# Kernel tuning notes

Hardware: AMD Instinct MI355X
Metric: run time of the kernel (lower is better)

The kernel has to match this reference:

```python
import jax, jax.numpy as jnp
import numpy as np

PS = 14            # patch size
EMBED = 1024       # vision embed dim
LLM = 2048         # llm embed dim
DS = 2             # downsample factor
B = 8
GRID = 64          # H = W = 64 patches per image
MAX_POS = 4096
ROPE_THETA = 10000.0


def _rope_cache(dim, max_pos, base):
    inv_freq = 1.0 / (base ** (jnp.arange(0, dim, 2, dtype=jnp.float32) / dim))
    t = jnp.arange(max_pos, dtype=jnp.float32)
    freqs = jnp.outer(t, inv_freq)  # [max_pos, dim//2]
    return jnp.cos(freqs), jnp.sin(freqs)


def setup_inputs() -> dict:
    key = jax.random.key(0)
    ks = jax.random.split(key, 5)
    n_total = B * GRID * GRID
    pixel_values = jax.random.normal(ks[0], (n_total, 3, PS, PS), jnp.float32)
    patch_w = jax.random.normal(ks[1], (EMBED, 3, PS, PS), jnp.float32) * (1.0 / np.sqrt(3 * PS * PS))
    patch_b = jax.random.normal(ks[2], (EMBED,), jnp.float32) * 0.02
    dense_w = jax.random.normal(ks[3], (LLM, EMBED, DS, DS), jnp.float32) * (1.0 / np.sqrt(EMBED * DS * DS))
    dense_b = jax.random.normal(ks[4], (LLM,), jnp.float32) * 0.02
    rope_dim = EMBED // 2
    cos_x, sin_x = _rope_cache(rope_dim, MAX_POS, ROPE_THETA)
    cos_y, sin_y = _rope_cache(rope_dim, MAX_POS, ROPE_THETA)
    grid_hw = jnp.full((B, 2), GRID, dtype=jnp.int32)
    return {"pixel_values": pixel_values, "grid_hw": grid_hw,
            "patch_w": patch_w, "patch_b": patch_b,
            "dense_w": dense_w, "dense_b": dense_b,
            "cos_x": cos_x, "sin_x": sin_x, "cos_y": cos_y, "sin_y": sin_y}


def _apply_rotary_1d(x, cos_c, sin_c, pos):
    # x: [N, d], cos_c/sin_c: [max_pos, d//2], pos: [N] int
    c = cos_c[pos]  # gather: [N, d//2]
    s = sin_c[pos]
    x1 = x[:, 0::2]
    x2 = x[:, 1::2]
    o1 = x1 * c - x2 * s
    o2 = x1 * s + x2 * c
    return jnp.stack([o1, o2], axis=-1).reshape(x.shape)  # re-interleave


def _positions(grid_np):
    # grid metadata is static host-side data; build per-patch (x, y) coords
    xs, ys = [], []
    for h, w in grid_np:
        pid = np.arange(h * w)
        xs.append(pid % w)
        ys.append(pid // w)
    return jnp.asarray(np.concatenate(xs)), jnp.asarray(np.concatenate(ys))


def reference(pixel_values, grid_hw, patch_w, patch_b, dense_w, dense_b,
              cos_x, sin_x, cos_y, sin_y):
    grid_np = np.asarray(grid_hw)
    # patchify conv (kernel == stride == patch) is a per-patch linear proj
    pe = jnp.einsum('nchw,echw->ne', pixel_values, patch_w) + patch_b  # [N, E]
    pe = jax.nn.gelu(pe, approximate=False)
    abs_x, abs_y = _positions(grid_np)
    half = EMBED // 2
    p1 = _apply_rotary_1d(pe[:, :half], cos_x, sin_x, abs_x)
    p2 = _apply_rotary_1d(pe[:, half:], cos_y, sin_y, abs_y)
    pe = jnp.concatenate([p1, p2], axis=-1)  # [N, E]
    # per-image downsample conv (kernel == stride == DS): 2x2 block linear
    outs = []
    cur = 0
    for h, w in grid_np:
        x = pe[cur:cur + h * w].reshape(h // DS, DS, w // DS, DS, EMBED)
        o = jnp.einsum('hpwqe,oepq->hwo', x, dense_w) + dense_b
        outs.append(o.reshape(-1, LLM))
        cur += h * w
    return jnp.concatenate(outs, axis=0)
```

## Files before the change

kernel.cpp:

```cpp
#include <hip/hip_runtime.h>
#include <cstdint>


using f16x8 = __attribute__((ext_vector_type(8))) _Float16;
using f32x4 = __attribute__((ext_vector_type(4))) float;

__device__ __forceinline__ void gload_lds16(const void* g, void* l) {
  __builtin_amdgcn_global_load_lds(
      reinterpret_cast<const __attribute__((address_space(1))) unsigned int*>(
          reinterpret_cast<uintptr_t>(g)),
      reinterpret_cast<__attribute__((address_space(3))) unsigned int*>(
          reinterpret_cast<uintptr_t>(l)),
      16, 0, 0);
}

__device__ __forceinline__ f16x8 ldsr(unsigned addr) {
  f16x8 r;
  asm volatile("ds_read_b128 %0, %1" : "=v"(r) : "v"(addr));
  return r;
}


#define KP 640

__global__ void conv_b1_kernel(const float* __restrict__ w1,
                               _Float16* __restrict__ h) {
  int i = blockIdx.x * 256 + threadIdx.x;
  if (i >= 1024 * KP) return;
  int e = i / KP;
  int k = i - e * KP;
  float v = (k < 588) ? w1[(size_t)e * 588 + k] : 0.0f;
  h[i] = (_Float16)v;
}

__global__ void conv_b2_kernel(const float* __restrict__ w2,
                               _Float16* __restrict__ h) {
  int i = blockIdx.x * 256 + threadIdx.x;
  int o   = i >> 12;
  int rem = i & 4095;
  int pq  = rem >> 10;
  int e   = rem & 1023;
  h[i] = (_Float16)w2[(size_t)o * 4096 + e * 4 + pq];
}

__global__ void conv_pix_kernel(const float* __restrict__ pix,
                                _Float16* __restrict__ h) {
  int i = blockIdx.x * 256 + threadIdx.x;
  if (i >= 32768 * (KP / 8)) return;
  int n = i / (KP / 8);
  int g = i - n * (KP / 8);
  int k0 = g * 8;
  f16x8 v;
  if (k0 + 8 <= 588) {
    const float4 x0 = *(const float4*)(pix + (size_t)n * 588 + k0);
    const float4 x1 = *(const float4*)(pix + (size_t)n * 588 + k0 + 4);
    v[0] = (_Float16)x0.x; v[1] = (_Float16)x0.y;
    v[2] = (_Float16)x0.z; v[3] = (_Float16)x0.w;
    v[4] = (_Float16)x1.x; v[5] = (_Float16)x1.y;
    v[6] = (_Float16)x1.z; v[7] = (_Float16)x1.w;
  } else {
#pragma unroll
    for (int j = 0; j < 8; ++j) {
      int k = k0 + j;
      v[j] = (k < 588) ? (_Float16)pix[(size_t)n * 588 + k] : (_Float16)0.0f;
    }
  }
  *(f16x8*)(h + (size_t)n * KP + k0) = v;
}


#define BAR   asm volatile("s_barrier" ::: "memory")
#define LGKM0 do { asm volatile("s_waitcnt lgkmcnt(0)" ::: "memory");         \
                   __builtin_amdgcn_sched_barrier(0); } while (0)
#define V6  asm volatile("s_waitcnt vmcnt(6)" ::: "memory")
#define V4  asm volatile("s_waitcnt vmcnt(4)" ::: "memory")
#define V0  asm volatile("s_waitcnt vmcnt(0)" ::: "memory")
#define VN  ((void)0)

#define MM16(I0, J0, AV, BV)                                                  \
  _Pragma("unroll") for (int i_ = 0; i_ < 4; ++i_)                            \
  _Pragma("unroll") for (int j_ = 0; j_ < 2; ++j_)                            \
  _Pragma("unroll") for (int ks_ = 0; ks_ < 2; ++ks_)                         \
      acc[(I0) + i_][(J0) + j_] = __builtin_amdgcn_mfma_f32_16x16x32_f16(     \
          AV[i_][ks_], BV[j_][ks_], acc[(I0) + i_][(J0) + j_], 0, 0, 0);

#define TILE_ITER(s, DOA, DOB, STGA, STGB, DRA, DRB, DRC, DRD)                \
  {                                                                           \
    const unsigned dbase = base + ((unsigned)((s) & 1) << 16);                \
    f16x8 av[4][2], vb0[2][2], vb1[2][2];                                     \
                                                       \
    _Pragma("unroll") for (int i = 0; i < 4; ++i) {                           \
      av[i][0] = ldsr(dbase + aoffs + (unsigned)(i * 2048) + soff0);          \
      av[i][1] = ldsr(dbase + aoffs + (unsigned)(i * 2048) + soff1);          \
    }                                                                         \
    _Pragma("unroll") for (int j = 0; j < 2; ++j) {                           \
      vb0[j][0] = ldsr(dbase + boffs + (unsigned)(j * 2048) + soff0);         \
      vb0[j][1] = ldsr(dbase + boffs + (unsigned)(j * 2048) + soff1);         \
    }                                                                         \
    if (DOA) STGA(0, (s) + 1);                                                \
    BAR; LGKM0;                                                               \
    __builtin_amdgcn_s_setprio(1);                                            \
    MM16(0, 0, av, vb0);                                                      \
    __builtin_amdgcn_s_setprio(0);                                            \
    DRA; BAR;                                                                 \
                                                       \
    _Pragma("unroll") for (int j = 0; j < 2; ++j) {                           \
      vb1[j][0] = ldsr(dbase + boffs + (unsigned)((2 + j) * 2048) + soff0);   \
      vb1[j][1] = ldsr(dbase + boffs + (unsigned)((2 + j) * 2048) + soff1);   \
    }                                                                         \
    if (DOA) STGA(1, (s) + 1);                                                \
    BAR; LGKM0;                                                               \
    __builtin_amdgcn_s_setprio(1);                                            \
    MM16(0, 2, av, vb1);                                                      \
    __builtin_amdgcn_s_setprio(0);                                            \
    DRB; BAR;                                                                 \
                                                       \
    _Pragma("unroll") for (int i = 0; i < 4; ++i) {                           \
      av[i][0] = ldsr(dbase + aoffs + (unsigned)((4 + i) * 2048) + soff0);    \
      av[i][1] = ldsr(dbase + aoffs + (unsigned)((4 + i) * 2048) + soff1);    \
    }                                                                         \
    if (DOB) STGB(0, (s) + 2);                                                \
    BAR; LGKM0;                                                               \
    __builtin_amdgcn_s_setprio(1);                                            \
    MM16(4, 2, av, vb1);                                                      \
    __builtin_amdgcn_s_setprio(0);                                            \
    DRC; BAR;                                                                 \
                                                       \
    if (DOB) STGB(1, (s) + 2);                                                \
    BAR;                                                                      \
    __builtin_amdgcn_s_setprio(1);                                            \
    MM16(4, 0, av, vb0);                                                      \
    __builtin_amdgcn_s_setprio(0);                                            \
    DRD; BAR;                                                                 \
  }


#define P_STGA(h, s)                                                          \
  _Pragma("unroll") for (int u = 0; u < 2; ++u) {                             \
    const int ibase = wave * 64 + u * 512;                                    \
    const int i = ibase + lane;                                               \
    const int row = i >> 3;                                                   \
    const int m = bm256 + (h) * 128 + row;                                    \
    const int gcol = (i & 7) ^ (row & 7);                                     \
    gload_lds16(pixf + (size_t)m * KP + (s) * 64 + gcol * 8,                  \
                (char*)lds + (((s) & 1) * 65536 + (h) * 16384 + ibase * 16)); \
  }
#define P_STGB(h, s)                                                          \
  _Pragma("unroll") for (int u = 0; u < 2; ++u) {                             \
    const int ibase = wave * 64 + u * 512;                                    \
    const int i = ibase + lane;                                               \
    const int row = i >> 3;                                                   \
    const int e = bn * 256 + (h) * 128 + row;                                 \
    const int gcol = (i & 7) ^ (row & 7);                                     \
    gload_lds16(b1w + (size_t)e * KP + (s) * 64 + gcol * 8,                   \
                (char*)lds + (((s) & 1) * 65536 + (2 + (h)) * 16384 +         \
                              ibase * 16));                                   \
  }

__global__ __launch_bounds__(512, 2) void patch_gemm8(
    const _Float16* __restrict__ pixf,
    const _Float16* __restrict__ b1w,
    const float* __restrict__ bias1,
    const float* __restrict__ cosx, const float* __restrict__ sinx,
    const float* __restrict__ cosy, const float* __restrict__ siny,
    _Float16* __restrict__ pe)
{
  __shared__ _Float16 lds[2][4][128][64];

  const int tid  = threadIdx.x;
  const int lane = tid & 63;
  const int wave = tid >> 6;
  const int wm = wave >> 2;
  const int wn = wave & 3;
  const int bm = blockIdx.x, bn = blockIdx.y;
  const int l15 = lane & 15;
  const int g   = lane >> 4;
  const int s7  = l15 & 7;

  const unsigned base  = (unsigned)(uintptr_t)&lds[0][0][0][0];
  const unsigned aoffs = (unsigned)(wm * 16384 + l15 * 128);
  const unsigned boffs = (unsigned)(32768 + (wn >> 1) * 16384 +
                                    (wn & 1) * 8192 + l15 * 128);
  const unsigned soff0 = (unsigned)(((0 + g) ^ s7) * 16);
  const unsigned soff1 = (unsigned)(((4 + g) ^ s7) * 16);

  const int bm256 = bm * 256;

  f32x4 acc[8][4] = {};

  P_STGA(0, 0); P_STGA(1, 0); P_STGB(0, 0); P_STGB(1, 0);
  P_STGB(0, 1); P_STGB(1, 1);
  V0; BAR;

  for (int kt = 0; kt < 8; ++kt)
    TILE_ITER(kt, 1, 1, P_STGA, P_STGB, V6, V6, V6, V4);
  TILE_ITER(8, 1, 0, P_STGA, P_STGB, V6, V6, V6, V0);
  TILE_ITER(9, 0, 0, P_STGA, P_STGB, VN, VN, VN, VN);

  const int md = (lane >> 4) * 4;
#pragma unroll
  for (int mf = 0; mf < 8; ++mf) {
#pragma unroll
    for (int r = 0; r < 4; ++r) {
      const int m = bm256 + wm * 128 + mf * 16 + md + r;
      const int pid  = m & 4095;
      const int posx = pid & 63;
      const int posy = (pid >> 6) & 63;
#pragma unroll
      for (int nf = 0; nf < 4; ++nf) {
        const int e = bn * 256 + wn * 64 + nf * 16 + l15;
        float v = acc[mf][nf][r] + bias1[e];
        v = 0.5f * v * (1.0f + erff(v * 0.70710678118654752f));
        const float pv = __shfl_xor(v, 1, 64);
        const int h2  = (e >= 512) ? 1 : 0;
        const int idx = (h2 ? (e - 512) : e) >> 1;
        const int pos = h2 ? posy : posx;
        const float cc = (h2 ? cosy : cosx)[pos * 256 + idx];
        const float ss = (h2 ? siny : sinx)[pos * 256 + idx];
        const float o = ((lane & 1) == 0) ? (v * cc - pv * ss)
                                          : (pv * ss + v * cc);
        pe[(size_t)m * 1024 + e] = (_Float16)o;
      }
    }
  }
}


#define D_STGA(h, s)                                                          \
  {                                                                           \
    const int pq = (s) >> 4, p = pq >> 1, q = pq & 1;                         \
    const int e0 = ((s) & 15) << 6;                                           \
    _Pragma("unroll") for (int u = 0; u < 2; ++u) {                           \
      const int ibase = wave * 64 + u * 512;                                  \
      const int i = ibase + lane;                                             \
      const int row = i >> 3;                                                 \
      const int t_ = bm256 + (h) * 128 + row;                                 \
      const int rr = t_ & 1023;                                               \
      const int prow =                                                        \
          (t_ >> 10) * 4096 + ((rr >> 5) * 2 + p) * 64 + (rr & 31) * 2 + q;   \
      const int gcol = (i & 7) ^ (row & 7);                                   \
      gload_lds16(pe + (size_t)prow * 1024 + e0 + gcol * 8,                   \
                  (char*)lds + (((s) & 1) * 65536 + (h) * 16384 +             \
                                ibase * 16));                                 \
    }                                                                         \
  }
#define D_STGB(h, s)                                                          \
  _Pragma("unroll") for (int u = 0; u < 2; ++u) {                             \
    const int ibase = wave * 64 + u * 512;                                    \
    const int i = ibase + lane;                                               \
    const int row = i >> 3;                                                   \
    const int n = bn * 256 + (h) * 128 + row;                                 \
    const int gcol = (i & 7) ^ (row & 7);                                     \
    gload_lds16(b2w + (size_t)n * 4096 + (s) * 64 + gcol * 8,                 \
                (char*)lds + (((s) & 1) * 65536 + (2 + (h)) * 16384 +         \
                              ibase * 16));                                   \
  }

__global__ __launch_bounds__(512, 2) void dense_gemm8(
    const _Float16* __restrict__ pe,
    const _Float16* __restrict__ b2w,
    const float* __restrict__ bias2, float* __restrict__ out)
{
  __shared__ _Float16 lds[2][4][128][64];

  const int tid  = threadIdx.x;
  const int lane = tid & 63;
  const int wave = tid >> 6;
  const int wm = wave >> 2;
  const int wn = wave & 3;
  const int f   = blockIdx.x;
  const int swz = (f & 7) * 32 + (f >> 3);
  const int bm  = swz & 31;
  const int bn  = swz >> 5;
  const int l15 = lane & 15;
  const int g   = lane >> 4;
  const int s7  = l15 & 7;

  const unsigned base  = (unsigned)(uintptr_t)&lds[0][0][0][0];
  const unsigned aoffs = (unsigned)(wm * 16384 + l15 * 128);
  const unsigned boffs = (unsigned)(32768 + (wn >> 1) * 16384 +
                                    (wn & 1) * 8192 + l15 * 128);
  const unsigned soff0 = (unsigned)(((0 + g) ^ s7) * 16);
  const unsigned soff1 = (unsigned)(((4 + g) ^ s7) * 16);

  const int bm256 = bm * 256;

  f32x4 acc[8][4] = {};

  D_STGA(0, 0); D_STGA(1, 0); D_STGB(0, 0); D_STGB(1, 0);
  D_STGB(0, 1); D_STGB(1, 1);
  V0; BAR;

  for (int kt = 0; kt < 62; ++kt)
    TILE_ITER(kt, 1, 1, D_STGA, D_STGB, V6, V6, V6, V4);
  TILE_ITER(62, 1, 0, D_STGA, D_STGB, V6, V6, V6, V0);
  TILE_ITER(63, 0, 0, D_STGA, D_STGB, VN, VN, VN, VN);

  const int md = (lane >> 4) * 4;
  const int r0 = bm256 + wm * 128;
  const int c0 = bn * 256 + wn * 64;
#pragma unroll
  for (int nf = 0; nf < 4; ++nf) {
    const int o = c0 + nf * 16 + l15;
    const float bs = bias2[o];
#pragma unroll
    for (int mf = 0; mf < 8; ++mf) {
      const int t_ = r0 + mf * 16 + md;
#pragma unroll
      for (int r = 0; r < 4; ++r)
        out[(size_t)(t_ + r) * 2048 + o] = acc[mf][nf][r] + bs;
    }
  }
}


extern "C" void kernel_launch(void* const* d_in, const int* in_sizes, int n_in,
                              void* d_out, int out_size, void* d_ws, size_t ws_size,
                              hipStream_t stream) {
  const float* pix  = (const float*)d_in[0];
  const float* w1   = (const float*)d_in[2];
  const float* b1   = (const float*)d_in[3];
  const float* w2   = (const float*)d_in[4];
  const float* b2   = (const float*)d_in[5];
  const float* cosx = (const float*)d_in[6];
  const float* sinx = (const float*)d_in[7];
  const float* cosy = (const float*)d_in[8];
  const float* siny = (const float*)d_in[9];
  float* out = (float*)d_out;

  _Float16* ws = (_Float16*)d_ws;
  const size_t PE_N  = (size_t)32768 * 1024;
  const size_t B1_N  = (size_t)1024 * KP;
  const size_t B2_N  = (size_t)2048 * 4096;
  _Float16* peb  = ws;
  _Float16* b1h  = peb + PE_N;
  _Float16* b2h  = b1h + B1_N;
  _Float16* pixf = b2h + B2_N;

  conv_b1_kernel<<<dim3((1024 * KP + 255) / 256), dim3(256), 0, stream>>>(w1, b1h);
  conv_b2_kernel<<<dim3(32768), dim3(256), 0, stream>>>(w2, b2h);
  conv_pix_kernel<<<dim3((32768 * (KP / 8) + 255) / 256), dim3(256), 0, stream>>>(pix, pixf);
  patch_gemm8<<<dim3(128, 4), dim3(512), 0, stream>>>(
      pixf, b1h, b1, cosx, sinx, cosy, siny, peb);
  dense_gemm8<<<dim3(256), dim3(512), 0, stream>>>(
      peb, b2h, b2, out);
}
```

Before: 303.1 us.

## Simplify GEMM pipelines and write patch embeddings in dense-gemm layout

Both GEMM kernels drop the hand-scheduled four-phase loop with partial vmcnt waits and interleaved staging. They now use a simple double-buffered loop that issues the next stage's loads, runs all MFMAs, then does a full wait and barrier. The patch GEMM epilogue scatters its output straight into the 2x2-downsample layout ([token][pq*1024+e]), so the dense GEMM reads A contiguously instead of through gathered row indices. The dense grid's block swizzle is removed as well. The loss of fine-grained load/compute overlap and L2-friendly block ordering may outweigh the cheaper addressing.

Result: faster. 290.8 us (-4.1%).

```diff
diff --git a/kernel.cpp b/kernel.cpp
--- a/kernel.cpp
+++ b/kernel.cpp
@@ -14,14 +14,12 @@
       16, 0, 0);
 }
 
-__device__ __forceinline__ f16x8 ldsr(unsigned addr) {
-  f16x8 r;
-  asm volatile("ds_read_b128 %0, %1" : "=v"(r) : "v"(addr));
-  return r;
-}
-
+#define BAR   asm volatile("s_barrier" ::: "memory")
+#define LGKM0 asm volatile("s_waitcnt lgkmcnt(0)" ::: "memory")
+#define VM0   asm volatile("s_waitcnt vmcnt(0)" ::: "memory")
 
 #define KP 640
+
 
 __global__ void conv_b1_kernel(const float* __restrict__ w1,
                                _Float16* __restrict__ h) {
@@ -69,133 +67,96 @@
 }
 
 
-#define BAR   asm volatile("s_barrier" ::: "memory")
-#define LGKM0 do { asm volatile("s_waitcnt lgkmcnt(0)" ::: "memory");         \
-                   __builtin_amdgcn_sched_barrier(0); } while (0)
-#define V6  asm volatile("s_waitcnt vmcnt(6)" ::: "memory")
-#define V4  asm volatile("s_waitcnt vmcnt(4)" ::: "memory")
-#define V0  asm volatile("s_waitcnt vmcnt(0)" ::: "memory")
-#define VN  ((void)0)
-
-#define MM16(I0, J0, AV, BV)                                                  \
+#define MFMA16(I0, J0, AV, BV)                                                \
   _Pragma("unroll") for (int i_ = 0; i_ < 4; ++i_)                            \
   _Pragma("unroll") for (int j_ = 0; j_ < 2; ++j_)                            \
-  _Pragma("unroll") for (int ks_ = 0; ks_ < 2; ++ks_)                         \
+  _Pragma("unroll") for (int k_ = 0; k_ < 2; ++k_)                            \
       acc[(I0) + i_][(J0) + j_] = __builtin_amdgcn_mfma_f32_16x16x32_f16(     \
-          AV[i_][ks_], BV[j_][ks_], acc[(I0) + i_][(J0) + j_], 0, 0, 0);
-
-#define TILE_ITER(s, DOA, DOB, STGA, STGB, DRA, DRB, DRC, DRD)                \
+          AV[i_][k_], BV[j_][k_], acc[(I0) + i_][(J0) + j_], 0, 0, 0);
+
+#define TILE_BODY(sb)                                                         \
   {                                                                           \
-    const unsigned dbase = base + ((unsigned)((s) & 1) << 16);                \
-    f16x8 av[4][2], vb0[2][2], vb1[2][2];                                     \
-                                                       \
+    f16x8 a0[4][2], a1[4][2], vb0[2][2], vb1[2][2];                           \
     _Pragma("unroll") for (int i = 0; i < 4; ++i) {                           \
-      av[i][0] = ldsr(dbase + aoffs + (unsigned)(i * 2048) + soff0);          \
-      av[i][1] = ldsr(dbase + aoffs + (unsigned)(i * 2048) + soff1);          \
+      a0[i][0] = *(const f16x8*)(lbase + (sb) + aoff + i * 2048 + so0);       \
+      a0[i][1] = *(const f16x8*)(lbase + (sb) + aoff + i * 2048 + so1);       \
     }                                                                         \
     _Pragma("unroll") for (int j = 0; j < 2; ++j) {                           \
-      vb0[j][0] = ldsr(dbase + boffs + (unsigned)(j * 2048) + soff0);         \
-      vb0[j][1] = ldsr(dbase + boffs + (unsigned)(j * 2048) + soff1);         \
-    }                                                                         \
-    if (DOA) STGA(0, (s) + 1);                                                \
-    BAR; LGKM0;                                                               \
-    __builtin_amdgcn_s_setprio(1);                                            \
-    MM16(0, 0, av, vb0);                                                      \
-    __builtin_amdgcn_s_setprio(0);                                            \
-    DRA; BAR;                                                                 \
-                                                       \
+      vb0[j][0] = *(const f16x8*)(lbase + (sb) + boff + j * 2048 + so0);      \
+      vb0[j][1] = *(const f16x8*)(lbase + (sb) + boff + j * 2048 + so1);      \
+    }                                                                         \
+    MFMA16(0, 0, a0, vb0);                                                    \
     _Pragma("unroll") for (int j = 0; j < 2; ++j) {                           \
-      vb1[j][0] = ldsr(dbase + boffs + (unsigned)((2 + j) * 2048) + soff0);   \
-      vb1[j][1] = ldsr(dbase + boffs + (unsigned)((2 + j) * 2048) + soff1);   \
-    }                                                                         \
-    if (DOA) STGA(1, (s) + 1);                                                \
-    BAR; LGKM0;                                                               \
-    __builtin_amdgcn_s_setprio(1);                                            \
-    MM16(0, 2, av, vb1);                                                      \
-    __builtin_amdgcn_s_setprio(0);                                            \
-    DRB; BAR;                                                                 \
-                                                       \
+      vb1[j][0] = *(const f16x8*)(lbase + (sb) + boff + (2+j) * 2048 + so0);  \
+      vb1[j][1] = *(const f16x8*)(lbase + (sb) + boff + (2+j) * 2048 + so1);  \
+    }                                                                         \
+    MFMA16(0, 2, a0, vb1);                                                    \
     _Pragma("unroll") for (int i = 0; i < 4; ++i) {                           \
-      av[i][0] = ldsr(dbase + aoffs + (unsigned)((4 + i) * 2048) + soff0);    \
-      av[i][1] = ldsr(dbase + aoffs + (unsigned)((4 + i) * 2048) + soff1);    \
-    }                                                                         \
-    if (DOB) STGB(0, (s) + 2);                                                \
-    BAR; LGKM0;                                                               \
-    __builtin_amdgcn_s_setprio(1);                                            \
-    MM16(4, 2, av, vb1);                                                      \
-    __builtin_amdgcn_s_setprio(0);                                            \
-    DRC; BAR;                                                                 \
-                                                       \
-    if (DOB) STGB(1, (s) + 2);                                                \
-    BAR;                                                                      \
-    __builtin_amdgcn_s_setprio(1);                                            \
-    MM16(4, 0, av, vb0);                                                      \
-    __builtin_amdgcn_s_setprio(0);                                            \
-    DRD; BAR;                                                                 \
-  }
-
-
-#define P_STGA(h, s)                                                          \
-  _Pragma("unroll") for (int u = 0; u < 2; ++u) {                             \
-    const int ibase = wave * 64 + u * 512;                                    \
-    const int i = ibase + lane;                                               \
-    const int row = i >> 3;                                                   \
-    const int m = bm256 + (h) * 128 + row;                                    \
-    const int gcol = (i & 7) ^ (row & 7);                                     \
-    gload_lds16(pixf + (size_t)m * KP + (s) * 64 + gcol * 8,                  \
-                (char*)lds + (((s) & 1) * 65536 + (h) * 16384 + ibase * 16)); \
-  }
-#define P_STGB(h, s)                                                          \
-  _Pragma("unroll") for (int u = 0; u < 2; ++u) {                             \
-    const int ibase = wave * 64 + u * 512;                                    \
-    const int i = ibase + lane;                                               \
-    const int row = i >> 3;                                                   \
-    const int e = bn * 256 + (h) * 128 + row;                                 \
-    const int gcol = (i & 7) ^ (row & 7);                                     \
-    gload_lds16(b1w + (size_t)e * KP + (s) * 64 + gcol * 8,                   \
-                (char*)lds + (((s) & 1) * 65536 + (2 + (h)) * 16384 +         \
-                              ibase * 16));                                   \
-  }
-
-__global__ __launch_bounds__(512, 2) void patch_gemm8(
+      a1[i][0] = *(const f16x8*)(lbase + (sb) + aoff + (4+i) * 2048 + so0);   \
+      a1[i][1] = *(const f16x8*)(lbase + (sb) + aoff + (4+i) * 2048 + so1);   \
+    }                                                                         \
+    MFMA16(4, 2, a1, vb1);                                                    \
+    MFMA16(4, 0, a1, vb0);                                                    \
+  }
+
+
+__global__ __launch_bounds__(512, 2) void patch_gemm9(
     const _Float16* __restrict__ pixf,
     const _Float16* __restrict__ b1w,
     const float* __restrict__ bias1,
     const float* __restrict__ cosx, const float* __restrict__ sinx,
     const float* __restrict__ cosy, const float* __restrict__ siny,
-    _Float16* __restrict__ pe)
+    _Float16* __restrict__ peM)
 {
-  __shared__ _Float16 lds[2][4][128][64];
+  __shared__ _Float16 lds[2][2][256][64];
 
   const int tid  = threadIdx.x;
   const int lane = tid & 63;
   const int wave = tid >> 6;
-  const int wm = wave >> 2;
-  const int wn = wave & 3;
+  const int wm = wave >> 2, wn = wave & 3;
   const int bm = blockIdx.x, bn = blockIdx.y;
   const int l15 = lane & 15;
   const int g   = lane >> 4;
   const int s7  = l15 & 7;
 
-  const unsigned base  = (unsigned)(uintptr_t)&lds[0][0][0][0];
-  const unsigned aoffs = (unsigned)(wm * 16384 + l15 * 128);
-  const unsigned boffs = (unsigned)(32768 + (wn >> 1) * 16384 +
-                                    (wn & 1) * 8192 + l15 * 128);
-  const unsigned soff0 = (unsigned)(((0 + g) ^ s7) * 16);
-  const unsigned soff1 = (unsigned)(((4 + g) ^ s7) * 16);
-
-  const int bm256 = bm * 256;
+  const char* lbase = (const char*)lds;
+  char*       lw    = (char*)lds;
+  const unsigned aoff = (unsigned)(wm * 16384 + l15 * 128);
+  const unsigned boff = (unsigned)(32768 + wn * 8192 + l15 * 128);
+  const unsigned so0  = (unsigned)(((0 + g) ^ s7) * 16);
+  const unsigned so1  = (unsigned)(((4 + g) ^ s7) * 16);
+
+  const int bm256 = bm * 256, bn256 = bn * 256;
+  const int srow = (wave * 4) * 8 + (lane >> 3);
+  const int sgc  = (lane & 7) ^ (srow & 7);
+
+  auto STAGE = [&](int s) {
+    char* slot = lw + ((size_t)(s & 1) << 16);
+    const int c0 = s * 64;
+#pragma unroll
+    for (int u = 0; u < 4; ++u) {
+      const int row  = srow + u * 8;
+      const int gcol = (lane & 7) ^ (row & 7);
+      gload_lds16(pixf + (size_t)(bm256 + row) * KP + c0 + gcol * 8,
+                  slot + (wave * 4 + u) * 1024);
+      gload_lds16(b1w + (size_t)(bn256 + row) * KP + c0 + gcol * 8,
+                  slot + 32768 + (wave * 4 + u) * 1024);
+    }
+  };
+  (void)sgc;
 
   f32x4 acc[8][4] = {};
 
-  P_STGA(0, 0); P_STGA(1, 0); P_STGB(0, 0); P_STGB(1, 0);
-  P_STGB(0, 1); P_STGB(1, 1);
-  V0; BAR;
-
-  for (int kt = 0; kt < 8; ++kt)
-    TILE_ITER(kt, 1, 1, P_STGA, P_STGB, V6, V6, V6, V4);
-  TILE_ITER(8, 1, 0, P_STGA, P_STGB, V6, V6, V6, V0);
-  TILE_ITER(9, 0, 0, P_STGA, P_STGB, VN, VN, VN, VN);
+  STAGE(0); VM0; BAR;
+#pragma unroll 2
+  for (int s = 0; s < 10; ++s) {
+    if (s + 1 < 10) STAGE(s + 1);
+    const unsigned sb = (unsigned)((s & 1) << 16);
+    __builtin_amdgcn_s_setprio(1);
+    TILE_BODY(sb);
+    __builtin_amdgcn_s_setprio(0);
+    LGKM0; VM0; BAR;
+  }
 
   const int md = (lane >> 4) * 4;
 #pragma unroll
@@ -204,101 +165,86 @@
     for (int r = 0; r < 4; ++r) {
       const int m = bm256 + wm * 128 + mf * 16 + md + r;
       const int pid  = m & 4095;
-      const int posx = pid & 63;
-      const int posy = (pid >> 6) & 63;
+      const int yy = pid >> 6, xx = pid & 63;
+      const int t  = (m >> 12) * 1024 + (yy >> 1) * 32 + (xx >> 1);
+      const int pq = (yy & 1) * 2 + (xx & 1);
+      _Float16* dst = peM + (size_t)t * 4096 + pq * 1024;
 #pragma unroll
       for (int nf = 0; nf < 4; ++nf) {
-        const int e = bn * 256 + wn * 64 + nf * 16 + l15;
+        const int e = bn256 + wn * 64 + nf * 16 + l15;
         float v = acc[mf][nf][r] + bias1[e];
         v = 0.5f * v * (1.0f + erff(v * 0.70710678118654752f));
         const float pv = __shfl_xor(v, 1, 64);
         const int h2  = (e >= 512) ? 1 : 0;
         const int idx = (h2 ? (e - 512) : e) >> 1;
-        const int pos = h2 ? posy : posx;
+        const int pos = h2 ? ((pid >> 6) & 63) : (pid & 63);
         const float cc = (h2 ? cosy : cosx)[pos * 256 + idx];
         const float ss = (h2 ? siny : sinx)[pos * 256 + idx];
         const float o = ((lane & 1) == 0) ? (v * cc - pv * ss)
                                           : (pv * ss + v * cc);
-        pe[(size_t)m * 1024 + e] = (_Float16)o;
+        dst[e] = (_Float16)o;
       }
     }
   }
 }
 
 
-#define D_STGA(h, s)                                                          \
-  {                                                                           \
-    const int pq = (s) >> 4, p = pq >> 1, q = pq & 1;                         \
-    const int e0 = ((s) & 15) << 6;                                           \
-    _Pragma("unroll") for (int u = 0; u < 2; ++u) {                           \
-      const int ibase = wave * 64 + u * 512;                                  \
-      const int i = ibase + lane;                                             \
-      const int row = i >> 3;                                                 \
-      const int t_ = bm256 + (h) * 128 + row;                                 \
-      const int rr = t_ & 1023;                                               \
-      const int prow =                                                        \
-          (t_ >> 10) * 4096 + ((rr >> 5) * 2 + p) * 64 + (rr & 31) * 2 + q;   \
-      const int gcol = (i & 7) ^ (row & 7);                                   \
-      gload_lds16(pe + (size_t)prow * 1024 + e0 + gcol * 8,                   \
-                  (char*)lds + (((s) & 1) * 65536 + (h) * 16384 +             \
-                                ibase * 16));                                 \
-    }                                                                         \
-  }
-#define D_STGB(h, s)                                                          \
-  _Pragma("unroll") for (int u = 0; u < 2; ++u) {                             \
-    const int ibase = wave * 64 + u * 512;                                    \
-    const int i = ibase + lane;                                               \
-    const int row = i >> 3;                                                   \
-    const int n = bn * 256 + (h) * 128 + row;                                 \
-    const int gcol = (i & 7) ^ (row & 7);                                     \
-    gload_lds16(b2w + (size_t)n * 4096 + (s) * 64 + gcol * 8,                 \
-                (char*)lds + (((s) & 1) * 65536 + (2 + (h)) * 16384 +         \
-                              ibase * 16));                                   \
-  }
-
-__global__ __launch_bounds__(512, 2) void dense_gemm8(
-    const _Float16* __restrict__ pe,
-    const _Float16* __restrict__ b2w,
+__global__ __launch_bounds__(512, 2) void dense_gemm9(
+    const _Float16* __restrict__ aM,
+    const _Float16* __restrict__ bM,
     const float* __restrict__ bias2, float* __restrict__ out)
 {
-  __shared__ _Float16 lds[2][4][128][64];
+  __shared__ _Float16 lds[2][2][256][64];
 
   const int tid  = threadIdx.x;
   const int lane = tid & 63;
   const int wave = tid >> 6;
-  const int wm = wave >> 2;
-  const int wn = wave & 3;
-  const int f   = blockIdx.x;
-  const int swz = (f & 7) * 32 + (f >> 3);
-  const int bm  = swz & 31;
-  const int bn  = swz >> 5;
+  const int wm = wave >> 2, wn = wave & 3;
+  const int bm = blockIdx.x, bn = blockIdx.y;
   const int l15 = lane & 15;
   const int g   = lane >> 4;
   const int s7  = l15 & 7;
 
-  const unsigned base  = (unsigned)(uintptr_t)&lds[0][0][0][0];
-  const unsigned aoffs = (unsigned)(wm * 16384 + l15 * 128);
-  const unsigned boffs = (unsigned)(32768 + (wn >> 1) * 16384 +
-                                    (wn & 1) * 8192 + l15 * 128);
-  const unsigned soff0 = (unsigned)(((0 + g) ^ s7) * 16);
-  const unsigned soff1 = (unsigned)(((4 + g) ^ s7) * 16);
-
-  const int bm256 = bm * 256;
+  const char* lbase = (const char*)lds;
+  char*       lw    = (char*)lds;
+  const unsigned aoff = (unsigned)(wm * 16384 + l15 * 128);
+  const unsigned boff = (unsigned)(32768 + wn * 8192 + l15 * 128);
+  const unsigned so0  = (unsigned)(((0 + g) ^ s7) * 16);
+  const unsigned so1  = (unsigned)(((4 + g) ^ s7) * 16);
+
+  const int bm256 = bm * 256, bn256 = bn * 256;
+  const int srow = (wave * 4) * 8 + (lane >> 3);
+
+  auto STAGE = [&](int s) {
+    char* slot = lw + ((size_t)(s & 1) << 16);
+    const int c0 = s * 64;
+#pragma unroll
+    for (int u = 0; u < 4; ++u) {
+      const int row  = srow + u * 8;
+      const int gcol = (lane & 7) ^ (row & 7);
+      gload_lds16(aM + (size_t)(bm256 + row) * 4096 + c0 + gcol * 8,
+                  slot + (wave * 4 + u) * 1024);
+      gload_lds16(bM + (size_t)(bn256 + row) * 4096 + c0 + gcol * 8,
+                  slot + 32768 + (wave * 4 + u) * 1024);
+    }
+  };
 
   f32x4 acc[8][4] = {};
 
-  D_STGA(0, 0); D_STGA(1, 0); D_STGB(0, 0); D_STGB(1, 0);
-  D_STGB(0, 1); D_STGB(1, 1);
-  V0; BAR;
-
-  for (int kt = 0; kt < 62; ++kt)
-    TILE_ITER(kt, 1, 1, D_STGA, D_STGB, V6, V6, V6, V4);
-  TILE_ITER(62, 1, 0, D_STGA, D_STGB, V6, V6, V6, V0);
-  TILE_ITER(63, 0, 0, D_STGA, D_STGB, VN, VN, VN, VN);
+  STAGE(0); VM0; BAR;
+#pragma unroll 2
+  for (int s = 0; s < 64; ++s) {
+    if (s + 1 < 64) STAGE(s + 1);
+    const unsigned sb = (unsigned)((s & 1) << 16);
+    __builtin_amdgcn_s_setprio(1);
+    TILE_BODY(sb);
+    __builtin_amdgcn_s_setprio(0);
+    LGKM0; VM0; BAR;
+  }
 
   const int md = (lane >> 4) * 4;
   const int r0 = bm256 + wm * 128;
-  const int c0 = bn * 256 + wn * 64;
+  const int c0 = bn256 + wn * 64;
 #pragma unroll
   for (int nf = 0; nf < 4; ++nf) {
     const int o = c0 + nf * 16 + l15;
@@ -329,19 +275,19 @@
   float* out = (float*)d_out;
 
   _Float16* ws = (_Float16*)d_ws;
-  const size_t PE_N  = (size_t)32768 * 1024;
+  const size_t PE_N  = (size_t)8192 * 4096;
   const size_t B1_N  = (size_t)1024 * KP;
   const size_t B2_N  = (size_t)2048 * 4096;
-  _Float16* peb  = ws;
-  _Float16* b1h  = peb + PE_N;
+  _Float16* peM  = ws;
+  _Float16* b1h  = peM + PE_N;
   _Float16* b2h  = b1h + B1_N;
   _Float16* pixf = b2h + B2_N;
 
   conv_b1_kernel<<<dim3((1024 * KP + 255) / 256), dim3(256), 0, stream>>>(w1, b1h);
   conv_b2_kernel<<<dim3(32768), dim3(256), 0, stream>>>(w2, b2h);
   conv_pix_kernel<<<dim3((32768 * (KP / 8) + 255) / 256), dim3(256), 0, stream>>>(pix, pixf);
-  patch_gemm8<<<dim3(128, 4), dim3(512), 0, stream>>>(
-      pixf, b1h, b1, cosx, sinx, cosy, siny, peb);
-  dense_gemm8<<<dim3(256), dim3(512), 0, stream>>>(
-      peb, b2h, b2, out);
-}
+  patch_gemm9<<<dim3(128, 4), dim3(512), 0, stream>>>(
+      pixf, b1h, b1, cosx, sinx, cosy, siny, peM);
+  dense_gemm9<<<dim3(32, 8), dim3(512), 0, stream>>>(
+      peM, b2h, b2, out);
+}
```
